# Performance work log

Hardware: AMD Instinct MI355X
Metric: run time of the kernel (lower is better)

Reference implementation:

```python
import jax, jax.numpy as jnp
import numpy as np

B, T, D, U, P, E = 32, 10, 10, 50, 50, 256
EPS_ATTN = 1e-8
EPS_LN = 1e-5


def _layer_norm(x, w, b):
    mu = jnp.mean(x, axis=-1, keepdims=True)
    var = jnp.mean((x - mu) ** 2, axis=-1, keepdims=True)
    return (x - mu) / jnp.sqrt(var + EPS_LN) * w + b


def setup_inputs() -> dict:
    key = jax.random.key(0)
    ks = jax.random.split(key, 8)
    xavier = float(np.sqrt(2.0 / (E + E)))
    return {
        "Q": jax.random.normal(ks[0], (B, T, U, E), dtype=jnp.float32),
        "K": jax.random.normal(ks[1], (B, D, P, E), dtype=jnp.float32),
        "V": jax.random.normal(ks[2], (B, D, P, E), dtype=jnp.float32),
        "attention_mask": jnp.zeros((B, T, D, U, P), dtype=jnp.float32),
        "W1": jax.random.normal(ks[3], (E, E), dtype=jnp.float32) * xavier,
        "b1": jnp.zeros((E,), dtype=jnp.float32),
        "W2": jax.random.normal(ks[4], (E, E), dtype=jnp.float32) * xavier,
        "b2": jnp.zeros((E,), dtype=jnp.float32),
        "ln1_w": jnp.ones((E,), dtype=jnp.float32),
        "ln1_b": jnp.zeros((E,), dtype=jnp.float32),
        "ln2_w": jnp.ones((E,), dtype=jnp.float32),
        "ln2_b": jnp.zeros((E,), dtype=jnp.float32),
    }


def reference(Q, K, V, attention_mask, W1, b1, W2, b2, ln1_w, ln1_b, ln2_w, ln2_b):
    # dk = max(1.0, emb_dim); scale = sqrt(dk) + eps
    scale = jnp.sqrt(jnp.asarray(float(max(1.0, Q.shape[-1])), dtype=Q.dtype)) + EPS_ATTN
    # (B,T,D,U,P) attention logits
    qk = jnp.einsum("btue,bdpe->btdup", Q, K) / scale + attention_mask
    score = jax.nn.softmax(qk, axis=-1)
    v_att = jnp.einsum("btdup,bdpe->btdue", score, V)  # (B,T,D,U,E)
    x = Q[:, :, None, :, :] + v_att  # broadcast over doc dim
    x = _layer_norm(x, ln1_w, ln1_b)
    ffn = jnp.maximum(x @ W1.T + b1, 0.0) @ W2.T + b2
    return _layer_norm(ffn + x, ln2_w, ln2_b)
```

## Files before the change

kernel.cpp:

```cpp
#include <hip/hip_runtime.h>
#include <math.h>

#define Bsz 32
#define Tt  10
#define Dd  10
#define Uu  50
#define Pp  50
#define Ee  256

typedef __attribute__((ext_vector_type(8))) short bf16x8;
typedef __attribute__((ext_vector_type(4))) float f32x4;

#define STK 264
#define STV 72
#define STS 72

#define OFF_A 0
#define OFF_B 36864
#define OFF_C 46080
#define SMEM_TOT 48128

__device__ __forceinline__ unsigned short f2bf(float f) {
    unsigned u = __builtin_bit_cast(unsigned, f);
    u += 0x7fffu + ((u >> 16) & 1u);
    return (unsigned short)(u >> 16);
}
__device__ __forceinline__ float bf2f(unsigned short h) {
    unsigned u = ((unsigned)h) << 16;
    return __builtin_bit_cast(float, u);
}
__device__ __forceinline__ bf16x8 ldfrag(const unsigned short* p, int stride, int r0, int c0, int lane) {
    return *(const bf16x8*)(p + (size_t)(r0 + (lane & 15)) * stride + c0 + ((lane >> 4) << 3));
}
__device__ __forceinline__ bf16x8 wfrag(const unsigned short* wbf, const float* wf, int use_ws,
                                        int n, int k0, int lane) {
    const int row = n + (lane & 15);
    const int col = k0 + ((lane >> 4) << 3);
    if (use_ws) {
        return *(const bf16x8*)(wbf + (size_t)row * 256 + col);
    }
    const float4 a = *(const float4*)(wf + (size_t)row * 256 + col);
    const float4 b = *(const float4*)(wf + (size_t)row * 256 + col + 4);
    bf16x8 r;
    r[0] = (short)f2bf(a.x); r[1] = (short)f2bf(a.y); r[2] = (short)f2bf(a.z); r[3] = (short)f2bf(a.w);
    r[4] = (short)f2bf(b.x); r[5] = (short)f2bf(b.y); r[6] = (short)f2bf(b.z); r[7] = (short)f2bf(b.w);
    return r;
}

__global__ void convert_w_kernel(const float* __restrict__ W1, const float* __restrict__ W2,
                                 unsigned short* __restrict__ ws) {
    int i4 = (blockIdx.x * 256 + threadIdx.x) * 4;
    float4 a = *(const float4*)(W1 + i4);
    ushort4 oa; oa.x = f2bf(a.x); oa.y = f2bf(a.y); oa.z = f2bf(a.z); oa.w = f2bf(a.w);
    *(ushort4*)(ws + i4) = oa;
    float4 b = *(const float4*)(W2 + i4);
    ushort4 ob; ob.x = f2bf(b.x); ob.y = f2bf(b.y); ob.z = f2bf(b.z); ob.w = f2bf(b.w);
    *(ushort4*)(ws + 65536 + i4) = ob;
}

__global__ __launch_bounds__(512, 6) void fusion_kernel(
    const float* __restrict__ Q,  const float* __restrict__ K,
    const float* __restrict__ V,  const float* __restrict__ Msk,
    const float* __restrict__ W1, const float* __restrict__ b1,
    const float* __restrict__ W2, const float* __restrict__ b2,
    const float* __restrict__ ln1w, const float* __restrict__ ln1b,
    const float* __restrict__ ln2w, const float* __restrict__ ln2b,
    const unsigned short* __restrict__ wsbf, int use_ws,
    float* __restrict__ out)
{
    __shared__ __align__(16) unsigned char smem[SMEM_TOT];
    unsigned short* sK   = (unsigned short*)(smem + OFF_A);
    unsigned short* sVt  = (unsigned short*)(smem + OFF_A);
    unsigned short* sXbf = (unsigned short*)(smem + OFF_A);
    unsigned short* sH   = (unsigned short*)(smem + OFF_A);
    unsigned short* sS   = (unsigned short*)(smem + OFF_B);
    float*          red  = (float*)(smem + OFF_C);
    float*          red2 = (float*)(smem + OFF_C);

    const int tid  = threadIdx.x;
    const int lane = tid & 63;
    const int wave = tid >> 6;
    const int quad = lane >> 4;
    const int l15  = lane & 15;

    const int btd = ((blockIdx.x & 7) * 400) + (blockIdx.x >> 3);
    const int b   = btd / (Tt * Dd);
    const int rem = btd % (Tt * Dd);
    const int t   = rem / Dd;
    const int d   = rem % Dd;

    const float* Qb = Q + ((size_t)(b * Tt + t) * Uu) * Ee;
    const float* Kb = K + ((size_t)(b * Dd + d) * Pp) * Ee;
    const float* Vb = V + ((size_t)(b * Dd + d) * Pp) * Ee;
    const float* Mb = Msk + ((size_t)((b * Tt + t) * Dd + d) * Uu) * Pp;
    float*       Ob = out + ((size_t)((b * Tt + t) * Dd + d) * Uu) * Ee;

    for (int i = tid; i < 3200; i += 512) {
        int r = i >> 6, c4 = (i & 63) << 2;
        float4 k = *(const float4*)(Kb + r * Ee + c4);
        ushort4 ok; ok.x = f2bf(k.x); ok.y = f2bf(k.y); ok.z = f2bf(k.z); ok.w = f2bf(k.w);
        *(ushort4*)(sK + r * STK + c4) = ok;
    }
    for (int i = tid; i < 924; i += 512) {
        int r = 50 + i / 66, c = (i % 66) << 2;
        ushort4 z = {0, 0, 0, 0};
        *(ushort4*)(sK + r * STK + c) = z;
    }
    __syncthreads();

    if (wave < 4) {
        const int mt = wave;
        int arow = mt * 16 + l15; if (arow > 49) arow = 49;
        const float* qrow = Qb + (size_t)arow * Ee + (quad << 3);
        f32x4 acc[4];
        #pragma unroll
        for (int i = 0; i < 4; ++i) acc[i] = (f32x4){0.f, 0.f, 0.f, 0.f};
        #pragma unroll
        for (int k0 = 0; k0 < 256; k0 += 32) {
            float4 qa = *(const float4*)(qrow + k0);
            float4 qb = *(const float4*)(qrow + k0 + 4);
            bf16x8 a;
            a[0] = (short)f2bf(qa.x); a[1] = (short)f2bf(qa.y); a[2] = (short)f2bf(qa.z); a[3] = (short)f2bf(qa.w);
            a[4] = (short)f2bf(qb.x); a[5] = (short)f2bf(qb.y); a[6] = (short)f2bf(qb.z); a[7] = (short)f2bf(qb.w);
            #pragma unroll
            for (int nt = 0; nt < 4; ++nt) {
                bf16x8 bf = ldfrag(sK, STK, nt << 4, k0, lane);
                acc[nt] = __builtin_amdgcn_mfma_f32_16x16x32_bf16(a, bf, acc[nt], 0, 0, 0);
            }
        }
        float l[4][4];
        #pragma unroll
        for (int nt = 0; nt < 4; ++nt) {
            int p = (nt << 4) + l15;
            #pragma unroll
            for (int r = 0; r < 4; ++r) {
                int u = mt * 16 + (quad << 2) + r;
                float v = acc[nt][r] * 0.0625f;
                if (p < Pp) { if (u < Uu) v += Mb[u * Pp + p]; }
                else v = -1e30f;
                l[nt][r] = v;
            }
        }
        #pragma unroll
        for (int r = 0; r < 4; ++r) {
            float m = fmaxf(fmaxf(l[0][r], l[1][r]), fmaxf(l[2][r], l[3][r]));
            #pragma unroll
            for (int msk = 1; msk < 16; msk <<= 1) m = fmaxf(m, __shfl_xor(m, msk));
            float e0 = __expf(l[0][r] - m), e1 = __expf(l[1][r] - m);
            float e2 = __expf(l[2][r] - m), e3 = __expf(l[3][r] - m);
            float s = e0 + e1 + e2 + e3;
            #pragma unroll
            for (int msk = 1; msk < 16; msk <<= 1) s += __shfl_xor(s, msk);
            float inv = 1.0f / s;
            int u = mt * 16 + (quad << 2) + r;
            sS[u * STS +  0 + l15] = f2bf(e0 * inv);
            sS[u * STS + 16 + l15] = f2bf(e1 * inv);
            sS[u * STS + 32 + l15] = f2bf(e2 * inv);
            sS[u * STS + 48 + l15] = f2bf(e3 * inv);
        }
    }
    __syncthreads();

    for (int i = tid; i < 12800; i += 512) {
        int p = i >> 8, e = i & 255;
        sVt[e * STV + p] = f2bf(Vb[p * Ee + e]);
    }
    for (int i = tid; i < 3584; i += 512) {
        int p = 50 + (i >> 8), e = i & 255;
        sVt[e * STV + p] = 0;
    }
    __syncthreads();

    {
        const int mt = wave >> 1;
        const int nh = (wave & 1) << 7;
        f32x4 acc[8];
        #pragma unroll
        for (int i = 0; i < 8; ++i) acc[i] = (f32x4){0.f, 0.f, 0.f, 0.f};
        #pragma unroll
        for (int k0 = 0; k0 < 64; k0 += 32) {
            bf16x8 a = ldfrag(sS, STS, mt << 4, k0, lane);
            #pragma unroll
            for (int nt = 0; nt < 8; ++nt) {
                bf16x8 bf = ldfrag(sVt, STV, nh + (nt << 4), k0, lane);
                acc[nt] = __builtin_amdgcn_mfma_f32_16x16x32_bf16(a, bf, acc[nt], 0, 0, 0);
            }
        }
        float s1[4] = {0.f, 0.f, 0.f, 0.f}, s2[4] = {0.f, 0.f, 0.f, 0.f};
        #pragma unroll
        for (int nt = 0; nt < 8; ++nt) {
            int e = nh + (nt << 4) + l15;
            #pragma unroll
            for (int r = 0; r < 4; ++r) {
                int u = (mt << 4) + (quad << 2) + r;
                float x = 0.f;
                if (u < Uu) x = acc[nt][r] + Qb[(size_t)u * Ee + e];
                acc[nt][r] = x;
                s1[r] += x; s2[r] += x * x;
            }
        }
        #pragma unroll
        for (int msk = 1; msk < 16; msk <<= 1) {
            #pragma unroll
            for (int r = 0; r < 4; ++r) { s1[r] += __shfl_xor(s1[r], msk); s2[r] += __shfl_xor(s2[r], msk); }
        }
        if (l15 == 0) {
            #pragma unroll
            for (int r = 0; r < 4; ++r) {
                int u = (mt << 4) + (quad << 2) + r;
                red[u * 4 + (wave & 1) * 2 + 0] = s1[r];
                red[u * 4 + (wave & 1) * 2 + 1] = s2[r];
            }
        }
        __syncthreads();
        float mu[4], rstd[4];
        #pragma unroll
        for (int r = 0; r < 4; ++r) {
            int u = (mt << 4) + (quad << 2) + r;
            float sum = red[u * 4 + 0] + red[u * 4 + 2];
            float sq  = red[u * 4 + 1] + red[u * 4 + 3];
            mu[r] = sum * (1.0f / 256.0f);
            float var = sq * (1.0f / 256.0f) - mu[r] * mu[r];
            rstd[r] = rsqrtf(var + 1e-5f);
        }
        #pragma unroll
        for (int nt = 0; nt < 8; ++nt) {
            int e = nh + (nt << 4) + l15;
            float wv = ln1w[e], bv = ln1b[e];
            #pragma unroll
            for (int r = 0; r < 4; ++r) {
                int u = (mt << 4) + (quad << 2) + r;
                float o = (u < Uu) ? ((acc[nt][r] - mu[r]) * rstd[r] * wv + bv) : 0.f;
                sXbf[u * STK + e] = f2bf(o);
            }
        }
    }
    __syncthreads();

    const int mp = wave >> 2;
    const int nq = wave & 3;
    unsigned resid[2][4][2];
    {
        f32x4 acc2[2][4];
        #pragma unroll
        for (int mi = 0; mi < 2; ++mi)
            #pragma unroll
            for (int nt = 0; nt < 4; ++nt) acc2[mi][nt] = (f32x4){0.f, 0.f, 0.f, 0.f};
        float b1v[4];
        #pragma unroll
        for (int nt = 0; nt < 4; ++nt) b1v[nt] = b1[(nq << 6) + (nt << 4) + l15];
        #pragma unroll
        for (int k0 = 0; k0 < 256; k0 += 32) {
            bf16x8 a0 = ldfrag(sXbf, STK, (mp << 5),      k0, lane);
            bf16x8 a1 = ldfrag(sXbf, STK, (mp << 5) + 16, k0, lane);
            #pragma unroll
            for (int nt = 0; nt < 4; ++nt) {
                bf16x8 bf = wfrag(wsbf, W1, use_ws, (nq << 6) + (nt << 4), k0, lane);
                acc2[0][nt] = __builtin_amdgcn_mfma_f32_16x16x32_bf16(a0, bf, acc2[0][nt], 0, 0, 0);
                acc2[1][nt] = __builtin_amdgcn_mfma_f32_16x16x32_bf16(a1, bf, acc2[1][nt], 0, 0, 0);
            }
        }
        #pragma unroll
        for (int mi = 0; mi < 2; ++mi)
            #pragma unroll
            for (int nt = 0; nt < 4; ++nt) {
                int j = (nq << 6) + (nt << 4) + l15;
                #pragma unroll
                for (int rp = 0; rp < 2; ++rp) {
                    int u0 = (mp << 5) + (mi << 4) + (quad << 2) + rp * 2;
                    unsigned lo = sXbf[(size_t)u0 * STK + j];
                    unsigned hi = sXbf[(size_t)(u0 + 1) * STK + j];
                    resid[mi][nt][rp] = lo | (hi << 16);
                }
            }
        __syncthreads();
        #pragma unroll
        for (int mi = 0; mi < 2; ++mi)
            #pragma unroll
            for (int nt = 0; nt < 4; ++nt) {
                int j = (nq << 6) + (nt << 4) + l15;
                #pragma unroll
                for (int r = 0; r < 4; ++r) {
                    int u = (mp << 5) + (mi << 4) + (quad << 2) + r;
                    sH[u * STK + j] = f2bf(fmaxf(acc2[mi][nt][r] + b1v[nt], 0.f));
                }
            }
    }
    __syncthreads();

    {
        f32x4 acc2[2][4];
        #pragma unroll
        for (int mi = 0; mi < 2; ++mi)
            #pragma unroll
            for (int nt = 0; nt < 4; ++nt) acc2[mi][nt] = (f32x4){0.f, 0.f, 0.f, 0.f};
        float b2v[4], w2l[4], b2l[4];
        #pragma unroll
        for (int nt = 0; nt < 4; ++nt) {
            int j = (nq << 6) + (nt << 4) + l15;
            b2v[nt] = b2[j]; w2l[nt] = ln2w[j]; b2l[nt] = ln2b[j];
        }
        #pragma unroll
        for (int k0 = 0; k0 < 256; k0 += 32) {
            bf16x8 a0 = ldfrag(sH, STK, (mp << 5),      k0, lane);
            bf16x8 a1 = ldfrag(sH, STK, (mp << 5) + 16, k0, lane);
            #pragma unroll
            for (int nt = 0; nt < 4; ++nt) {
                bf16x8 bf = wfrag(wsbf + 65536, W2, use_ws, (nq << 6) + (nt << 4), k0, lane);
                acc2[0][nt] = __builtin_amdgcn_mfma_f32_16x16x32_bf16(a0, bf, acc2[0][nt], 0, 0, 0);
                acc2[1][nt] = __builtin_amdgcn_mfma_f32_16x16x32_bf16(a1, bf, acc2[1][nt], 0, 0, 0);
            }
        }
        float s1[2][4], s2[2][4];
        #pragma unroll
        for (int mi = 0; mi < 2; ++mi)
            #pragma unroll
            for (int r = 0; r < 4; ++r) { s1[mi][r] = 0.f; s2[mi][r] = 0.f; }
        #pragma unroll
        for (int mi = 0; mi < 2; ++mi)
            #pragma unroll
            for (int nt = 0; nt < 4; ++nt) {
                #pragma unroll
                for (int r = 0; r < 4; ++r) {
                    unsigned pk = resid[mi][nt][r >> 1];
                    unsigned short rb = (r & 1) ? (unsigned short)(pk >> 16) : (unsigned short)(pk & 0xffffu);
                    float y = acc2[mi][nt][r] + b2v[nt] + bf2f(rb);
                    acc2[mi][nt][r] = y;
                    s1[mi][r] += y; s2[mi][r] += y * y;
                }
            }
        #pragma unroll
        for (int msk = 1; msk < 16; msk <<= 1)
            #pragma unroll
            for (int mi = 0; mi < 2; ++mi)
                #pragma unroll
                for (int r = 0; r < 4; ++r) {
                    s1[mi][r] += __shfl_xor(s1[mi][r], msk);
                    s2[mi][r] += __shfl_xor(s2[mi][r], msk);
                }
        if (l15 == 0) {
            #pragma unroll
            for (int mi = 0; mi < 2; ++mi)
                #pragma unroll
                for (int r = 0; r < 4; ++r) {
                    int u = (mp << 5) + (mi << 4) + (quad << 2) + r;
                    red2[u * 8 + nq * 2 + 0] = s1[mi][r];
                    red2[u * 8 + nq * 2 + 1] = s2[mi][r];
                }
        }
        __syncthreads();
        #pragma unroll
        for (int mi = 0; mi < 2; ++mi)
            #pragma unroll
            for (int r = 0; r < 4; ++r) {
                int u = (mp << 5) + (mi << 4) + (quad << 2) + r;
                if (u < Uu) {
                    float sum = red2[u * 8 + 0] + red2[u * 8 + 2] + red2[u * 8 + 4] + red2[u * 8 + 6];
                    float sq  = red2[u * 8 + 1] + red2[u * 8 + 3] + red2[u * 8 + 5] + red2[u * 8 + 7];
                    float mu = sum * (1.0f / 256.0f);
                    float var = sq * (1.0f / 256.0f) - mu * mu;
                    float rstd = rsqrtf(var + 1e-5f);
                    #pragma unroll
                    for (int nt = 0; nt < 4; ++nt) {
                        int j = (nq << 6) + (nt << 4) + l15;
                        Ob[(size_t)u * Ee + j] = (acc2[mi][nt][r] - mu) * rstd * w2l[nt] + b2l[nt];
                    }
                }
            }
    }
}

extern "C" void kernel_launch(void* const* d_in, const int* in_sizes, int n_in,
                              void* d_out, int out_size, void* d_ws, size_t ws_size,
                              hipStream_t stream) {
    const float* Q    = (const float*)d_in[0];
    const float* K    = (const float*)d_in[1];
    const float* V    = (const float*)d_in[2];
    const float* M    = (const float*)d_in[3];
    const float* W1   = (const float*)d_in[4];
    const float* b1   = (const float*)d_in[5];
    const float* W2   = (const float*)d_in[6];
    const float* b2   = (const float*)d_in[7];
    const float* ln1w = (const float*)d_in[8];
    const float* ln1b = (const float*)d_in[9];
    const float* ln2w = (const float*)d_in[10];
    const float* ln2b = (const float*)d_in[11];
    float* out = (float*)d_out;

    int use_ws = (ws_size >= 262144) ? 1 : 0;
    const unsigned short* wsbf = (const unsigned short*)d_ws;
    if (use_ws) {
        convert_w_kernel<<<64, 256, 0, stream>>>(W1, W2, (unsigned short*)d_ws);
    }
    fusion_kernel<<<Bsz * Tt * Dd, 512, 0, stream>>>(Q, K, V, M, W1, b1, W2, b2,
                                                     ln1w, ln1b, ln2w, ln2b,
                                                     wsbf, use_ws, out);
}
```

Baseline: 608.7 us.

## Overlap V transpose staging with QK^T by reading K fragments from global

The kernel no longer stages K into LDS. The four QK waves now build their bf16 B-fragments straight from global memory, clamping padded rows to row 49; those columns are masked to -1e30 afterwards. Meanwhile the other four waves transpose V into LDS, which removes one barrier and a serial staging phase. In exchange, each QK wave re-reads the whole K tile from global/L1 and does its own conversion, and the launch-bounds occupancy hint drops from 6 to 4, giving more registers but fewer resident blocks.

```diff
diff --git a/kernel.cpp b/kernel.cpp
--- a/kernel.cpp
+++ b/kernel.cpp
@@ -31,6 +31,17 @@
 }
 __device__ __forceinline__ bf16x8 ldfrag(const unsigned short* p, int stride, int r0, int c0, int lane) {
     return *(const bf16x8*)(p + (size_t)(r0 + (lane & 15)) * stride + c0 + ((lane >> 4) << 3));
+}
+__device__ __forceinline__ bf16x8 kfrag(const float* __restrict__ Kb, int n, int k0, int lane) {
+    int row = n + (lane & 15);
+    row = row > 49 ? 49 : row;
+    const int col = k0 + ((lane >> 4) << 3);
+    const float4 a = *(const float4*)(Kb + (size_t)row * 256 + col);
+    const float4 b = *(const float4*)(Kb + (size_t)row * 256 + col + 4);
+    bf16x8 r;
+    r[0] = (short)f2bf(a.x); r[1] = (short)f2bf(a.y); r[2] = (short)f2bf(a.z); r[3] = (short)f2bf(a.w);
+    r[4] = (short)f2bf(b.x); r[5] = (short)f2bf(b.y); r[6] = (short)f2bf(b.z); r[7] = (short)f2bf(b.w);
+    return r;
 }
 __device__ __forceinline__ bf16x8 wfrag(const unsigned short* wbf, const float* wf, int use_ws,
                                         int n, int k0, int lane) {
@@ -58,7 +69,7 @@
     *(ushort4*)(ws + 65536 + i4) = ob;
 }
 
-__global__ __launch_bounds__(512, 6) void fusion_kernel(
+__global__ __launch_bounds__(512, 4) void fusion_kernel(
     const float* __restrict__ Q,  const float* __restrict__ K,
     const float* __restrict__ V,  const float* __restrict__ Msk,
     const float* __restrict__ W1, const float* __restrict__ b1,
@@ -69,7 +80,6 @@
     float* __restrict__ out)
 {
     __shared__ __align__(16) unsigned char smem[SMEM_TOT];
-    unsigned short* sK   = (unsigned short*)(smem + OFF_A);
     unsigned short* sVt  = (unsigned short*)(smem + OFF_A);
     unsigned short* sXbf = (unsigned short*)(smem + OFF_A);
     unsigned short* sH   = (unsigned short*)(smem + OFF_A);
@@ -95,19 +105,6 @@
     const float* Mb = Msk + ((size_t)((b * Tt + t) * Dd + d) * Uu) * Pp;
     float*       Ob = out + ((size_t)((b * Tt + t) * Dd + d) * Uu) * Ee;
 
-    for (int i = tid; i < 3200; i += 512) {
-        int r = i >> 6, c4 = (i & 63) << 2;
-        float4 k = *(const float4*)(Kb + r * Ee + c4);
-        ushort4 ok; ok.x = f2bf(k.x); ok.y = f2bf(k.y); ok.z = f2bf(k.z); ok.w = f2bf(k.w);
-        *(ushort4*)(sK + r * STK + c4) = ok;
-    }
-    for (int i = tid; i < 924; i += 512) {
-        int r = 50 + i / 66, c = (i % 66) << 2;
-        ushort4 z = {0, 0, 0, 0};
-        *(ushort4*)(sK + r * STK + c) = z;
-    }
-    __syncthreads();
-
     if (wave < 4) {
         const int mt = wave;
         int arow = mt * 16 + l15; if (arow > 49) arow = 49;
@@ -124,7 +121,7 @@
             a[4] = (short)f2bf(qb.x); a[5] = (short)f2bf(qb.y); a[6] = (short)f2bf(qb.z); a[7] = (short)f2bf(qb.w);
             #pragma unroll
             for (int nt = 0; nt < 4; ++nt) {
-                bf16x8 bf = ldfrag(sK, STK, nt << 4, k0, lane);
+                bf16x8 bf = kfrag(Kb, nt << 4, k0, lane);
                 acc[nt] = __builtin_amdgcn_mfma_f32_16x16x32_bf16(a, bf, acc[nt], 0, 0, 0);
             }
         }
@@ -158,16 +155,17 @@
             sS[u * STS + 32 + l15] = f2bf(e2 * inv);
             sS[u * STS + 48 + l15] = f2bf(e3 * inv);
         }
-    }
-    __syncthreads();
-
-    for (int i = tid; i < 12800; i += 512) {
-        int p = i >> 8, e = i & 255;
-        sVt[e * STV + p] = f2bf(Vb[p * Ee + e]);
-    }
-    for (int i = tid; i < 3584; i += 512) {
-        int p = 50 + (i >> 8), e = i & 255;
-        sVt[e * STV + p] = 0;
+    } else {
+        const int lt = tid - 256;
+        #pragma unroll 4
+        for (int i = lt; i < 12800; i += 256) {
+            int p = i >> 8, e = i & 255;
+            sVt[e * STV + p] = f2bf(Vb[p * Ee + e]);
+        }
+        for (int i = lt; i < 3584; i += 256) {
+            int p = 50 + (i >> 8), e = i & 255;
+            sVt[e * STV + p] = 0;
+        }
     }
     __syncthreads();
 
```

Measured after the change: 588.9 us. 3.3% less time.
